# Kernel optimization log

Measured on AMD Instinct MI355X. Metric: run time of the kernel, lower is better.

The kernel has to match this reference:

```python
import jax, jax.numpy as jnp
import numpy as np

B, IN, N, D, O, H = 8192, 512, 16, 128, 256, 4
HD = D // H
PI = jnp.float32(np.pi)


def setup_inputs() -> dict:
    key = jax.random.key(0)
    ks = jax.random.split(key, 18)
    rn = lambda k, s, sc=1.0: jax.random.normal(k, s, dtype=jnp.float32) * sc
    return {
        'x': rn(ks[0], (B, IN)),
        'W_amp_r': rn(ks[1], (IN, N * D), 0.05), 'b_amp_r': rn(ks[2], (N * D,), 0.05),
        'W_amp_i': rn(ks[3], (IN, N * D), 0.05), 'b_amp_i': rn(ks[4], (N * D,), 0.05),
        'W_ph': rn(ks[5], (IN, N), 0.05), 'b_ph': rn(ks[6], (N,), 0.05),
        'A_param': rn(ks[7], (N, N), 0.01),
        'Wqkv_r': rn(ks[8], (D, 3 * D), 0.08), 'bqkv_r': rn(ks[9], (3 * D,), 0.08),
        'Wqkv_i': rn(ks[10], (D, 3 * D), 0.08), 'bqkv_i': rn(ks[11], (3 * D,), 0.08),
        'Wout_r': rn(ks[12], (D, D), 0.08), 'bout_r': rn(ks[13], (D,), 0.08),
        'Wout_i': rn(ks[14], (D, D), 0.08), 'bout_i': rn(ks[15], (D,), 0.08),
        'M_r': rn(ks[16], (N, D, O), 1.0 / np.sqrt(D)),
        'M_i': rn(ks[17], (N, D, O), 1.0 / np.sqrt(D)),
    }


def reference(x, W_amp_r, b_amp_r, W_amp_i, b_amp_i, W_ph, b_ph, A_param,
              Wqkv_r, bqkv_r, Wqkv_i, bqkv_i, Wout_r, bout_r, Wout_i, bout_i,
              M_r, M_i):
    # --- quantum phase encoding ---
    amp_r = (x @ W_amp_r + b_amp_r).reshape(B, N, D)
    amp_i = (x @ W_amp_i + b_amp_i).reshape(B, N, D)
    phases = jnp.tanh(x @ W_ph + b_ph) * PI                # (B, N)
    c, s = jnp.cos(phases)[..., None], jnp.sin(phases)[..., None]
    s_r = amp_r * c - amp_i * s
    s_i = amp_r * s + amp_i * c
    norm = jnp.sqrt(jnp.sum(s_r * s_r + s_i * s_i, -1, keepdims=True) + 1e-8)
    s_r, s_i = s_r / norm, s_i / norm
    # --- Cayley unitary interference ---
    A = (A_param - A_param.T).astype(jnp.complex64)
    I = jnp.eye(N, dtype=jnp.complex64)
    U = jnp.linalg.solve(I - 1j * A, I + 1j * A)           # (N, N) unitary
    st = (s_r + 1j * s_i).astype(jnp.complex64)
    interf = jnp.einsum('bmd,mn->bnd', st, U)
    sr, si = jnp.real(interf), jnp.imag(interf)
    # --- complex multi-head attention (magnitude softmax) ---
    scale = jnp.float32(HD ** -0.5)
    qkv_r = (sr @ Wqkv_r + bqkv_r).reshape(B, N, 3, H, HD).transpose(2, 0, 3, 1, 4)
    qkv_i = (si @ Wqkv_i + bqkv_i).reshape(B, N, 3, H, HD).transpose(2, 0, 3, 1, 4)
    q_r, k_r, v_r = qkv_r[0], qkv_r[1], qkv_r[2]
    q_i, k_i, v_i = qkv_i[0], qkv_i[1], qkv_i[2]
    ar = (jnp.einsum('bhnd,bhmd->bhnm', q_r, k_r) + jnp.einsum('bhnd,bhmd->bhnm', q_i, k_i)) * scale
    ai = (jnp.einsum('bhnd,bhmd->bhnm', q_i, k_r) - jnp.einsum('bhnd,bhmd->bhnm', q_r, k_i)) * scale
    w = jax.nn.softmax(jnp.sqrt(ar * ar + ai * ai), axis=-1)
    o_r = jnp.einsum('bhnm,bhmd->bhnd', w, v_r).transpose(0, 2, 1, 3).reshape(B, N, D)
    o_i = jnp.einsum('bhnm,bhmd->bhnd', w, v_i).transpose(0, 2, 1, 3).reshape(B, N, D)
    att_r = o_r @ Wout_r + bout_r
    att_i = o_i @ Wout_i + bout_i
    # --- quantum measurement ---
    m_r = jnp.einsum('bnd,ndo->bno', att_r, M_r) - jnp.einsum('bnd,ndo->bno', att_i, M_i)
    m_i = jnp.einsum('bnd,ndo->bno', att_r, M_i) + jnp.einsum('bnd,ndo->bno', att_i, M_r)
    probs = jax.nn.softmax(jnp.mean(jnp.sqrt(m_r * m_r + m_i * m_i), -1), axis=-1)  # (B, N)
    out_r = jnp.sum(m_r * probs[..., None], 1)
    out_i = jnp.sum(m_i * probs[..., None], 1)
    classical = jnp.sqrt(out_r * out_r + out_i * out_i)     # (B, O)
    # --- quantum metrics ---
    mag2 = sr * sr + si * si
    sum_sq = jnp.sum(mag2, -1)
    purity_bn = jnp.sum(mag2 * mag2, -1) / (sum_sq * sum_sq + 1e-8)
    purity_b = jnp.mean(purity_bn, -1)
    entanglement_b = -jnp.log(purity_b + 1e-8)
    fn = jnp.sqrt(jnp.sum(mag2, -1, keepdims=True) + 1e-8)
    nr, ni = sr / fn, si / fn
    Rij = jnp.einsum('bid,bjd->bij', nr, nr) + jnp.einsum('bid,bjd->bij', ni, ni)
    Iij = jnp.einsum('bid,bjd->bij', nr, ni) - jnp.einsum('bid,bjd->bij', ni, nr)
    fidelity = jnp.clip(Rij * Rij + Iij * Iij, 0.0, 1.0)    # (B, N, N), symmetric
    phase_var = jnp.mean(jnp.var(phases, axis=1, ddof=1))
    return (classical, probs, jnp.mean(att_r, 1), jnp.mean(att_i, 1),
            jnp.mean(purity_b), jnp.mean(entanglement_b), fidelity, phase_var)
```

## Files before the change

kernel.cpp:

```cpp
#include <hip/hip_runtime.h>
#include <math.h>

#define B_ 8192
#define IN_ 512
#define NQ 16
#define DD 128
#define OO 256
#define PI_F 3.14159274101257324f
#define INV_B (1.0f/8192.0f)
#define SCALE_F 0.176776695296636881f

#define OFF_CLASS 0
#define OFF_PROBS 2097152
#define OFF_ATTRM 2228224
#define OFF_ATTIM 3276800
#define OFF_PUR   4325376
#define OFF_ENT   4325377
#define OFF_FID   4325378
#define OFF_PV    6422530

__global__ __launch_bounds__(256) void cayley_kernel(const float* __restrict__ A_param,
                                                     float* __restrict__ Ur,
                                                     float* __restrict__ Ui) {
    __shared__ float Mr[16][17], Mi[16][17], Rr[16][17], Ri[16][17];
    const int t = threadIdx.x;
    const int r = t >> 4, c = t & 15;
    float a = A_param[r*16 + c] - A_param[c*16 + r];
    Mr[r][c] = (r == c) ? 1.0f : 0.0f;
    Mi[r][c] = -a;
    Rr[r][c] = (r == c) ? 1.0f : 0.0f;
    Ri[r][c] = a;
    __syncthreads();
    for (int p = 0; p < 16; p++) {
        float prr = Mr[p][p], pii = Mi[p][p];
        __syncthreads();
        if (r == p) {
            float inv = 1.0f / (prr*prr + pii*pii);
            float mr0 = Mr[p][c], mi0 = Mi[p][c];
            Mr[p][c] = (mr0*prr + mi0*pii) * inv;
            Mi[p][c] = (mi0*prr - mr0*pii) * inv;
            float rr0 = Rr[p][c], ri0 = Ri[p][c];
            Rr[p][c] = (rr0*prr + ri0*pii) * inv;
            Ri[p][c] = (ri0*prr - rr0*pii) * inv;
        }
        __syncthreads();
        float fr = Mr[r][p], fi = Mi[r][p];
        float mpr = Mr[p][c], mpi = Mi[p][c];
        float rpr = Rr[p][c], rpi = Ri[p][c];
        __syncthreads();
        if (r != p) {
            Mr[r][c] -= fr*mpr - fi*mpi;
            Mi[r][c] -= fr*mpi + fi*mpr;
            Rr[r][c] -= fr*rpr - fi*rpi;
            Ri[r][c] -= fr*rpi + fi*rpr;
        }
        __syncthreads();
    }
    Ur[t] = Rr[r][c];
    Ui[t] = Ri[r][c];
}

__global__ __launch_bounds__(256) void gemm_f32(const float* __restrict__ A, int lda,
                                                const float* __restrict__ W, int ldw,
                                                const float* __restrict__ bias,
                                                float* __restrict__ C, int ldc, int K) {
    __shared__ float As[32][132];
    __shared__ float Bs[32][132];
    const int t = threadIdx.x;
    const int tm = t >> 4, tn = t & 15;
    const size_t r0 = (size_t)blockIdx.x * 128;
    const int c0 = blockIdx.y * 128;
    float acc[8][8];
#pragma unroll
    for (int i = 0; i < 8; i++)
#pragma unroll
        for (int j = 0; j < 8; j++) acc[i][j] = 0.0f;

    for (int k0 = 0; k0 < K; k0 += 32) {
#pragma unroll
        for (int i = 0; i < 4; i++) {
            int idx = t + i*256;
            int mm = idx >> 3, kq = (idx & 7) << 2;
            float4 va = *(const float4*)&A[(r0 + mm)*lda + (k0 + kq)];
            As[kq+0][mm] = va.x; As[kq+1][mm] = va.y;
            As[kq+2][mm] = va.z; As[kq+3][mm] = va.w;
        }
#pragma unroll
        for (int i = 0; i < 4; i++) {
            int idx = t + i*256;
            int kk = idx >> 5, cq = (idx & 31) << 2;
            *(float4*)&Bs[kk][cq] = *(const float4*)&W[(size_t)(k0+kk)*ldw + (c0+cq)];
        }
        __syncthreads();
#pragma unroll
        for (int kk = 0; kk < 32; kk++) {
            float4 a0 = *(const float4*)&As[kk][tm*4];
            float4 a1 = *(const float4*)&As[kk][64 + tm*4];
            float4 b0 = *(const float4*)&Bs[kk][tn*4];
            float4 b1 = *(const float4*)&Bs[kk][64 + tn*4];
            float av[8] = {a0.x,a0.y,a0.z,a0.w,a1.x,a1.y,a1.z,a1.w};
            float bv[8] = {b0.x,b0.y,b0.z,b0.w,b1.x,b1.y,b1.z,b1.w};
#pragma unroll
            for (int i = 0; i < 8; i++)
#pragma unroll
                for (int j = 0; j < 8; j++)
                    acc[i][j] = fmaf(av[i], bv[j], acc[i][j]);
        }
        __syncthreads();
    }
#pragma unroll
    for (int ri = 0; ri < 2; ri++)
#pragma unroll
    for (int i = 0; i < 4; i++) {
        size_t row = r0 + ri*64 + tm*4 + i;
#pragma unroll
        for (int ci = 0; ci < 2; ci++) {
            int col = c0 + ci*64 + tn*4;
            float4 bb = *(const float4*)&bias[col];
            float4 v;
            v.x = acc[ri*4+i][ci*4+0] + bb.x;
            v.y = acc[ri*4+i][ci*4+1] + bb.y;
            v.z = acc[ri*4+i][ci*4+2] + bb.z;
            v.w = acc[ri*4+i][ci*4+3] + bb.w;
            *(float4*)&C[row*ldc + col] = v;
        }
    }
}

__global__ __launch_bounds__(256) void phases_kernel(const float* __restrict__ x,
                                                     const float* __restrict__ W_ph,
                                                     const float* __restrict__ b_ph,
                                                     float* __restrict__ phases) {
    __shared__ float xs[512];
    __shared__ float part[256];
    const int t = threadIdx.x;
    const size_t b = blockIdx.x;
    xs[t]       = x[b*512 + t];
    xs[t + 256] = x[b*512 + t + 256];
    __syncthreads();
    const int n2 = t & 15, g = t >> 4;
    float s = 0.0f;
#pragma unroll
    for (int j = 0; j < 32; j++) {
        int k = g*32 + j;
        s = fmaf(xs[k], W_ph[k*16 + n2], s);
    }
    part[t] = s;
    __syncthreads();
    if (t < 16) {
        float acc = b_ph[t];
#pragma unroll
        for (int g2 = 0; g2 < 16; g2++) acc += part[g2*16 + t];
        phases[b*16 + t] = tanhf(acc) * PI_F;
    }
}

__global__ __launch_bounds__(256) void mega_kernel(
    const float* ampR, const float* ampI,
    const float* __restrict__ phases,
    const float* __restrict__ Ur, const float* __restrict__ Ui,
    const float* __restrict__ Wqkv_r, const float* __restrict__ bqkv_r,
    const float* __restrict__ Wqkv_i, const float* __restrict__ bqkv_i,
    const float* __restrict__ Wout_r, const float* __restrict__ bout_r,
    const float* __restrict__ Wout_i, const float* __restrict__ bout_i,
    float* attR, float* attI,
    float* __restrict__ fid,
    float* __restrict__ attmR, float* __restrict__ attmI,
    float* __restrict__ pur_out, float* __restrict__ ent_out, float* __restrict__ pv_out)
{
    __shared__ float S[15808];
    float* br   = S;
    float* bi   = S + 2048;
    float* ir   = S + 4096;
    float* ii   = S + 6208;
    float* red  = S + 8320;
    float* red2 = S + 8576;
    float* csn  = S + 8832;
    float* snn  = S + 8848;
    float* invn = S + 8864;
    float* fnv  = S + 8880;
    float* purs = S + 8896;
    float* phl  = S + 8912;
    float* Urs  = S + 8928;
    float* Uis  = S + 9184;
    float* Wrc  = S + 9472;
    float* Wic  = S + 12544;
    float* qr2  = S;
    float* qi2  = S + 2112;
    float* kr2  = S + 4224;
    float* ki2  = S + 6336;
    float* vr2  = S + 8448;
    float* vi2  = S + 10560;
    float* wbuf = S + 12672;
    float* Wor  = S + 13760;
    float* Woi  = S + 14784;
    float* or_  = S;
    float* oi_  = S + 2112;
    float* attSr= S + 4224;
    float* attSi= S + 6336;

    const int t = threadIdx.x;
    const size_t b = blockIdx.x;

    {
        const float4* aR = (const float4*)(ampR + b*2048);
        const float4* aI = (const float4*)(ampI + b*2048);
#pragma unroll
        for (int i = 0; i < 2; i++) {
            int c = t + i*256;
            *(float4*)&br[c*4] = aR[c];
            *(float4*)&bi[c*4] = aI[c];
        }
    }
    Urs[t] = Ur[t]; Uis[t] = Ui[t];
    if (t < 16) {
        float p = phases[b*16 + t];
        phl[t] = p; csn[t] = cosf(p); snn[t] = sinf(p);
    }
    __syncthreads();
#pragma unroll
    for (int i = 0; i < 8; i++) {
        int idx = t + i*256;
        int n2 = idx >> 7;
        float ar = br[idx], ai = bi[idx];
        float cc = csn[n2], ss = snn[n2];
        br[idx] = ar*cc - ai*ss;
        bi[idx] = ar*ss + ai*cc;
    }
    __syncthreads();
    {
        const int n2 = t >> 4, g = t & 15;
        const float* pr  = &br[n2*128 + g*8];
        const float* pi2 = &bi[n2*128 + g*8];
        float s = 0.0f;
#pragma unroll
        for (int j = 0; j < 8; j++) s += pr[j]*pr[j] + pi2[j]*pi2[j];
        red[t] = s;
    }
    __syncthreads();
    if (t < 16) {
        float s = 0.0f;
#pragma unroll
        for (int g2 = 0; g2 < 16; g2++) s += red[t*16 + g2];
        invn[t] = 1.0f / sqrtf(s + 1e-8f);
    }
    __syncthreads();
#pragma unroll
    for (int i = 0; i < 8; i++) {
        int idx = t + i*256;
        float iv = invn[idx >> 7];
        br[idx] *= iv; bi[idx] *= iv;
    }
    __syncthreads();
#pragma unroll
    for (int rep = 0; rep < 8; rep++) {
        int o = t + rep*256;
        int n2 = o >> 7, d = o & 127;
        float ar = 0.0f, ai = 0.0f;
#pragma unroll
        for (int m = 0; m < 16; m++) {
            float vr = br[m*128 + d], vi = bi[m*128 + d];
            float ur = Urs[m*16 + n2], ui = Uis[m*16 + n2];
            ar += vr*ur - vi*ui;
            ai += vr*ui + vi*ur;
        }
        ir[n2*132 + d] = ar; ii[n2*132 + d] = ai;
    }
    __syncthreads();
    {
        const int n2 = t >> 4, g = t & 15;
        float s2 = 0.0f, s4 = 0.0f;
#pragma unroll
        for (int j = 0; j < 8; j++) {
            float xr = ir[n2*132 + g*8+j], xi = ii[n2*132 + g*8+j];
            float m2 = xr*xr + xi*xi;
            s2 += m2; s4 += m2*m2;
        }
        red[t] = s2; red2[t] = s4;
    }
    __syncthreads();
    if (t < 16) {
        float S2 = 0.0f, S4 = 0.0f;
#pragma unroll
        for (int g2 = 0; g2 < 16; g2++) { S2 += red[t*16+g2]; S4 += red2[t*16+g2]; }
        purs[t] = S4 / (S2*S2 + 1e-8f);
        fnv[t] = sqrtf(S2 + 1e-8f);
    }
    __syncthreads();
    if (t == 0) {
        float pb = 0.0f;
#pragma unroll
        for (int n2 = 0; n2 < 16; n2++) pb += purs[n2];
        pb *= (1.0f/16.0f);
        atomicAdd(pur_out, pb * INV_B);
        atomicAdd(ent_out, -logf(pb + 1e-8f) * INV_B);
    }
    if (t == 1) {
        float mean = 0.0f;
#pragma unroll
        for (int n2 = 0; n2 < 16; n2++) mean += phl[n2];
        mean *= (1.0f/16.0f);
        float var = 0.0f;
#pragma unroll
        for (int n2 = 0; n2 < 16; n2++) { float dv = phl[n2] - mean; var += dv*dv; }
        var *= (1.0f/15.0f);
        atomicAdd(pv_out, var * INV_B);
    }
    {
        const int i2 = t >> 4, j2 = t & 15;
        float Rt = 0.0f, It = 0.0f;
#pragma unroll
        for (int d0 = 0; d0 < 128; d0 += 4) {
            float4 xr = *(const float4*)&ir[i2*132 + d0];
            float4 xi = *(const float4*)&ii[i2*132 + d0];
            float4 yr = *(const float4*)&ir[j2*132 + d0];
            float4 yi = *(const float4*)&ii[j2*132 + d0];
            Rt += xr.x*yr.x + xi.x*yi.x;  It += xr.x*yi.x - xi.x*yr.x;
            Rt += xr.y*yr.y + xi.y*yi.y;  It += xr.y*yi.y - xi.y*yr.y;
            Rt += xr.z*yr.z + xi.z*yi.z;  It += xr.z*yi.z - xi.z*yr.z;
            Rt += xr.w*yr.w + xi.w*yi.w;  It += xr.w*yi.w - xi.w*yr.w;
        }
        float inv = 1.0f / (fnv[i2]*fnv[j2]);
        float F = (Rt*Rt + It*It) * inv * inv;
        F = fminf(fmaxf(F, 0.0f), 1.0f);
        fid[b*256 + t] = F;
    }

    const int cg = t >> 4, nn = t & 15;
    float aq[24], bq[24];
#pragma unroll
    for (int j = 0; j < 24; j++) { aq[j] = 0.0f; bq[j] = 0.0f; }
    for (int d0 = 0; d0 < 128; d0 += 8) {
        __syncthreads();
#pragma unroll
        for (int i = 0; i < 3; i++) {
            int idx = (t + i*256) * 4;
            *(float4*)&Wrc[idx] = *(const float4*)&Wqkv_r[d0*384 + idx];
            *(float4*)&Wic[idx] = *(const float4*)&Wqkv_i[d0*384 + idx];
        }
        __syncthreads();
#pragma unroll
        for (int dd = 0; dd < 8; dd++) {
            const float arr = ir[nn*132 + d0 + dd];
            const float aii = ii[nn*132 + d0 + dd];
#pragma unroll
            for (int s2 = 0; s2 < 6; s2++) {
                const float4 wr4 = *(const float4*)&Wrc[dd*384 + cg*4 + 64*s2];
                const float4 wi4 = *(const float4*)&Wic[dd*384 + cg*4 + 64*s2];
                aq[s2*4+0] = fmaf(arr, wr4.x, aq[s2*4+0]);
                aq[s2*4+1] = fmaf(arr, wr4.y, aq[s2*4+1]);
                aq[s2*4+2] = fmaf(arr, wr4.z, aq[s2*4+2]);
                aq[s2*4+3] = fmaf(arr, wr4.w, aq[s2*4+3]);
                bq[s2*4+0] = fmaf(aii, wi4.x, bq[s2*4+0]);
                bq[s2*4+1] = fmaf(aii, wi4.y, bq[s2*4+1]);
                bq[s2*4+2] = fmaf(aii, wi4.z, bq[s2*4+2]);
                bq[s2*4+3] = fmaf(aii, wi4.w, bq[s2*4+3]);
            }
        }
    }
    __syncthreads();
#pragma unroll
    for (int s2 = 0; s2 < 6; s2++) {
#pragma unroll
        for (int j = 0; j < 4; j++) {
            const int c = cg*4 + 64*s2 + j;
            float qvr = aq[s2*4+j] + bqkv_r[c];
            float qvi = bq[s2*4+j] + bqkv_i[c];
            if (s2 < 2)      { qr2[nn*132 + c]         = qvr; qi2[nn*132 + c]         = qvi; }
            else if (s2 < 4) { kr2[nn*132 + (c-128)]   = qvr; ki2[nn*132 + (c-128)]   = qvi; }
            else             { vr2[nn*132 + (c-256)]   = qvr; vi2[nn*132 + (c-256)]   = qvi; }
        }
    }
    __syncthreads();

    {
        const int nq = t >> 4, m = t & 15;
#pragma unroll
        for (int h = 0; h < 4; h++) {
            float ar = 0.0f, ai = 0.0f;
            const int bqo = h*32;
#pragma unroll
            for (int d0 = 0; d0 < 32; d0 += 4) {
                float4 q_r = *(const float4*)&qr2[nq*132 + bqo + d0];
                float4 k_r = *(const float4*)&kr2[m*132  + bqo + d0];
                float4 q_i = *(const float4*)&qi2[nq*132 + bqo + d0];
                float4 k_i = *(const float4*)&ki2[m*132  + bqo + d0];
                ar += q_r.x*k_r.x + q_i.x*k_i.x + q_r.y*k_r.y + q_i.y*k_i.y
                    + q_r.z*k_r.z + q_i.z*k_i.z + q_r.w*k_r.w + q_i.w*k_i.w;
                ai += q_i.x*k_r.x - q_r.x*k_i.x + q_i.y*k_r.y - q_r.y*k_i.y
                    + q_i.z*k_r.z - q_r.z*k_i.z + q_i.w*k_r.w - q_r.w*k_i.w;
            }
            wbuf[h*272 + nq*17 + m] = sqrtf(ar*ar + ai*ai) * SCALE_F;
        }
    }
    __syncthreads();
    if (t < 64) {
        const int h = t >> 4, n2 = t & 15;
        float* row = &wbuf[h*272 + n2*17];
        float mx = row[0];
#pragma unroll
        for (int k = 1; k < 16; k++) mx = fmaxf(mx, row[k]);
        float ev[16];
        float sum = 0.0f;
#pragma unroll
        for (int k = 0; k < 16; k++) { ev[k] = expf(row[k] - mx); sum += ev[k]; }
        float inv = 1.0f / sum;
#pragma unroll
        for (int k = 0; k < 16; k++) row[k] = ev[k] * inv;
    }
    __syncthreads();

    {
        const int og = t >> 4, n2 = t & 15;
        const int hh = og >> 2;
        float por[8] = {0,0,0,0,0,0,0,0}, poi[8] = {0,0,0,0,0,0,0,0};
#pragma unroll
        for (int m2 = 0; m2 < 16; m2++) {
            float w = wbuf[hh*272 + n2*17 + m2];
            float4 v0 = *(const float4*)&vr2[m2*132 + og*8];
            float4 v1 = *(const float4*)&vr2[m2*132 + og*8 + 4];
            float4 u0 = *(const float4*)&vi2[m2*132 + og*8];
            float4 u1 = *(const float4*)&vi2[m2*132 + og*8 + 4];
            por[0] = fmaf(w, v0.x, por[0]); por[1] = fmaf(w, v0.y, por[1]);
            por[2] = fmaf(w, v0.z, por[2]); por[3] = fmaf(w, v0.w, por[3]);
            por[4] = fmaf(w, v1.x, por[4]); por[5] = fmaf(w, v1.y, por[5]);
            por[6] = fmaf(w, v1.z, por[6]); por[7] = fmaf(w, v1.w, por[7]);
            poi[0] = fmaf(w, u0.x, poi[0]); poi[1] = fmaf(w, u0.y, poi[1]);
            poi[2] = fmaf(w, u0.z, poi[2]); poi[3] = fmaf(w, u0.w, poi[3]);
            poi[4] = fmaf(w, u1.x, poi[4]); poi[5] = fmaf(w, u1.y, poi[5]);
            poi[6] = fmaf(w, u1.z, poi[6]); poi[7] = fmaf(w, u1.w, poi[7]);
        }
#pragma unroll
        for (int j = 0; j < 8; j++) {
            or_[n2*132 + og*8 + j] = por[j];
            oi_[n2*132 + og*8 + j] = poi[j];
        }
    }
    __syncthreads();

    {
        const int og = t >> 4, n2 = t & 15;
        float atr[8] = {0,0,0,0,0,0,0,0}, ati[8] = {0,0,0,0,0,0,0,0};
        for (int d0 = 0; d0 < 128; d0 += 8) {
            __syncthreads();
            *(float4*)&Wor[t*4] = *(const float4*)&Wout_r[d0*128 + t*4];
            *(float4*)&Woi[t*4] = *(const float4*)&Wout_i[d0*128 + t*4];
            __syncthreads();
#pragma unroll
            for (int dd = 0; dd < 8; dd++) {
                const float a_r = or_[n2*132 + d0 + dd];
                const float a_i = oi_[n2*132 + d0 + dd];
                float4 w0 = *(const float4*)&Wor[dd*128 + og*8];
                float4 w1 = *(const float4*)&Wor[dd*128 + og*8 + 4];
                float4 u0 = *(const float4*)&Woi[dd*128 + og*8];
                float4 u1 = *(const float4*)&Woi[dd*128 + og*8 + 4];
                atr[0] = fmaf(a_r, w0.x, atr[0]); atr[1] = fmaf(a_r, w0.y, atr[1]);
                atr[2] = fmaf(a_r, w0.z, atr[2]); atr[3] = fmaf(a_r, w0.w, atr[3]);
                atr[4] = fmaf(a_r, w1.x, atr[4]); atr[5] = fmaf(a_r, w1.y, atr[5]);
                atr[6] = fmaf(a_r, w1.z, atr[6]); atr[7] = fmaf(a_r, w1.w, atr[7]);
                ati[0] = fmaf(a_i, u0.x, ati[0]); ati[1] = fmaf(a_i, u0.y, ati[1]);
                ati[2] = fmaf(a_i, u0.z, ati[2]); ati[3] = fmaf(a_i, u0.w, ati[3]);
                ati[4] = fmaf(a_i, u1.x, ati[4]); ati[5] = fmaf(a_i, u1.y, ati[5]);
                ati[6] = fmaf(a_i, u1.z, ati[6]); ati[7] = fmaf(a_i, u1.w, ati[7]);
            }
        }
        const float4 br0 = *(const float4*)&bout_r[og*8];
        const float4 br1 = *(const float4*)&bout_r[og*8 + 4];
        const float4 bi0 = *(const float4*)&bout_i[og*8];
        const float4 bi1 = *(const float4*)&bout_i[og*8 + 4];
        float4 o0 = make_float4(atr[0]+br0.x, atr[1]+br0.y, atr[2]+br0.z, atr[3]+br0.w);
        float4 o1 = make_float4(atr[4]+br1.x, atr[5]+br1.y, atr[6]+br1.z, atr[7]+br1.w);
        float4 e0 = make_float4(ati[0]+bi0.x, ati[1]+bi0.y, ati[2]+bi0.z, ati[3]+bi0.w);
        float4 e1 = make_float4(ati[4]+bi1.x, ati[5]+bi1.y, ati[6]+bi1.z, ati[7]+bi1.w);
        size_t gbase = b*2048 + (size_t)n2*128 + og*8;
        *(float4*)&attR[gbase]     = o0;
        *(float4*)&attR[gbase + 4] = o1;
        *(float4*)&attI[gbase]     = e0;
        *(float4*)&attI[gbase + 4] = e1;
        *(float4*)&attSr[n2*132 + og*8]     = o0;
        *(float4*)&attSr[n2*132 + og*8 + 4] = o1;
        *(float4*)&attSi[n2*132 + og*8]     = e0;
        *(float4*)&attSi[n2*132 + og*8 + 4] = e1;
    }
    __syncthreads();

    if (t < 128) {
        const int d = t;
        float s = 0.0f;
#pragma unroll
        for (int n2 = 0; n2 < 16; n2++) s += attSr[n2*132 + d];
        attmR[b*128 + d] = s * (1.0f/16.0f);
    } else {
        const int d = t - 128;
        float s = 0.0f;
#pragma unroll
        for (int n2 = 0; n2 < 16; n2++) s += attSi[n2*132 + d];
        attmI[b*128 + d] = s * (1.0f/16.0f);
    }
}

template<int MODE>
__global__ __launch_bounds__(256) void measure_kernel(const float* __restrict__ attR,
                                                      const float* __restrict__ attI,
                                                      const float* __restrict__ M_r,
                                                      const float* __restrict__ M_i,
                                                      float* __restrict__ mR,
                                                      float* __restrict__ mI,
                                                      float* __restrict__ mag,
                                                      const float* __restrict__ probs,
                                                      float* __restrict__ orAcc,
                                                      float* __restrict__ oiAcc) {
    __shared__ float ar_s[32*128];
    __shared__ float ai_s[32*128];
    const int t = threadIdx.x;
    const size_t b0 = (size_t)blockIdx.x * 32;
    const int n = blockIdx.y;
#pragma unroll
    for (int i = 0; i < 4; i++) {
        int c = t + i*256;
        int row = c >> 5, d4 = (c & 31) << 2;
        *(float4*)&ar_s[row*128 + d4] = *(const float4*)&attR[((b0+row)*16 + n)*128 + d4];
        *(float4*)&ai_s[row*128 + d4] = *(const float4*)&attI[((b0+row)*16 + n)*128 + d4];
    }
    __syncthreads();
    const int ol = t & 63;
    const int rg = t >> 6;
    const int obase = ol * 4;
    float mr[8][4], mi[8][4];
#pragma unroll
    for (int i = 0; i < 8; i++)
#pragma unroll
        for (int j = 0; j < 4; j++) { mr[i][j] = 0.0f; mi[i][j] = 0.0f; }
    const float* Mrp = M_r + (size_t)n*DD*OO;
    const float* Mip = M_i + (size_t)n*DD*OO;
    for (int k0 = 0; k0 < 128; k0 += 4) {
        float4 Mr4[4], Mi4[4];
#pragma unroll
        for (int u = 0; u < 4; u++) {
            Mr4[u] = *(const float4*)&Mrp[(k0+u)*256 + obase];
            Mi4[u] = *(const float4*)&Mip[(k0+u)*256 + obase];
        }
#pragma unroll
        for (int r8 = 0; r8 < 8; r8++) {
            const int row = rg*8 + r8;
            float4 a4 = *(const float4*)&ar_s[row*128 + k0];
            float4 c4 = *(const float4*)&ai_s[row*128 + k0];
            float arv[4] = {a4.x, a4.y, a4.z, a4.w};
            float aiv[4] = {c4.x, c4.y, c4.z, c4.w};
#pragma unroll
            for (int u = 0; u < 4; u++) {
                float ar = arv[u], ai = aiv[u];
                mr[r8][0] = fmaf(ar, Mr4[u].x, mr[r8][0]); mr[r8][0] = fmaf(-ai, Mi4[u].x, mr[r8][0]);
                mr[r8][1] = fmaf(ar, Mr4[u].y, mr[r8][1]); mr[r8][1] = fmaf(-ai, Mi4[u].y, mr[r8][1]);
                mr[r8][2] = fmaf(ar, Mr4[u].z, mr[r8][2]); mr[r8][2] = fmaf(-ai, Mi4[u].z, mr[r8][2]);
                mr[r8][3] = fmaf(ar, Mr4[u].w, mr[r8][3]); mr[r8][3] = fmaf(-ai, Mi4[u].w, mr[r8][3]);
                mi[r8][0] = fmaf(ar, Mi4[u].x, mi[r8][0]); mi[r8][0] = fmaf( ai, Mr4[u].x, mi[r8][0]);
                mi[r8][1] = fmaf(ar, Mi4[u].y, mi[r8][1]); mi[r8][1] = fmaf( ai, Mr4[u].y, mi[r8][1]);
                mi[r8][2] = fmaf(ar, Mi4[u].z, mi[r8][2]); mi[r8][2] = fmaf( ai, Mr4[u].z, mi[r8][2]);
                mi[r8][3] = fmaf(ar, Mi4[u].w, mi[r8][3]); mi[r8][3] = fmaf( ai, Mr4[u].w, mi[r8][3]);
            }
        }
    }
#pragma unroll
    for (int r8 = 0; r8 < 8; r8++) {
        const int row = rg*8 + r8;
        if constexpr (MODE == 0) {
            size_t base = ((b0+row)*16 + n)*256 + obase;
            *(float4*)&mR[base] = make_float4(mr[r8][0], mr[r8][1], mr[r8][2], mr[r8][3]);
            *(float4*)&mI[base] = make_float4(mi[r8][0], mi[r8][1], mi[r8][2], mi[r8][3]);
        }
        if constexpr (MODE == 2) {
            float p = probs[(b0+row)*16 + n];
            size_t abase = (b0+row)*256 + obase;
#pragma unroll
            for (int u = 0; u < 4; u++) {
                atomicAdd(&orAcc[abase + u], p * mr[r8][u]);
                atomicAdd(&oiAcc[abase + u], p * mi[r8][u]);
            }
        } else {
            float p = 0.0f;
#pragma unroll
            for (int u = 0; u < 4; u++)
                p += sqrtf(mr[r8][u]*mr[r8][u] + mi[r8][u]*mi[r8][u]);
#pragma unroll
            for (int s = 32; s > 0; s >>= 1) p += __shfl_down(p, s, 64);
            if (ol == 0) mag[(b0+row)*16 + n] = p * (1.0f/256.0f);
        }
    }
}

__global__ __launch_bounds__(256) void final_kernel(const float* __restrict__ mR,
                                                    const float* __restrict__ mI,
                                                    const float* __restrict__ mag,
                                                    float* __restrict__ cls,
                                                    float* __restrict__ probs) {
    __shared__ float pr[16];
    const size_t b = blockIdx.x;
    const int t = threadIdx.x;
    if (t == 0) {
        float v[16];
        float mx = -1e30f;
#pragma unroll
        for (int n2 = 0; n2 < 16; n2++) { v[n2] = mag[b*16 + n2]; mx = fmaxf(mx, v[n2]); }
        float sum = 0.0f;
#pragma unroll
        for (int n2 = 0; n2 < 16; n2++) { float e = expf(v[n2] - mx); pr[n2] = e; sum += e; }
        float inv = 1.0f / sum;
#pragma unroll
        for (int n2 = 0; n2 < 16; n2++) pr[n2] *= inv;
    }
    __syncthreads();
    if (t < 16) probs[b*16 + t] = pr[t];
    float orv = 0.0f, oiv = 0.0f;
#pragma unroll
    for (int n2 = 0; n2 < 16; n2++) {
        float p = pr[n2];
        size_t base = (b*16 + n2)*256 + t;
        orv = fmaf(mR[base], p, orv);
        oiv = fmaf(mI[base], p, oiv);
    }
    cls[b*256 + t] = sqrtf(orv*orv + oiv*oiv);
}

__global__ __launch_bounds__(256) void probs_kernel(const float* __restrict__ mag,
                                                    float* __restrict__ probs) {
    const int b = blockIdx.x*256 + threadIdx.x;
    float v[16];
    float mx = -1e30f;
#pragma unroll
    for (int n2 = 0; n2 < 16; n2++) { v[n2] = mag[b*16 + n2]; mx = fmaxf(mx, v[n2]); }
    float sum = 0.0f;
#pragma unroll
    for (int n2 = 0; n2 < 16; n2++) { v[n2] = expf(v[n2] - mx); sum += v[n2]; }
    float inv = 1.0f / sum;
#pragma unroll
    for (int n2 = 0; n2 < 16; n2++) probs[b*16 + n2] = v[n2] * inv;
}

__global__ __launch_bounds__(256) void classical_kernel(const float* __restrict__ orAcc,
                                                        const float* __restrict__ oiAcc,
                                                        float* __restrict__ cls) {
    const size_t i = (size_t)blockIdx.x*256 + threadIdx.x;
    float a = orAcc[i], c = oiAcc[i];
    cls[i] = sqrtf(a*a + c*c);
}

extern "C" void kernel_launch(void* const* d_in, const int* in_sizes, int n_in,
                              void* d_out, int out_size, void* d_ws, size_t ws_size,
                              hipStream_t stream) {
    const float* x        = (const float*)d_in[0];
    const float* W_amp_r  = (const float*)d_in[1];
    const float* b_amp_r  = (const float*)d_in[2];
    const float* W_amp_i  = (const float*)d_in[3];
    const float* b_amp_i  = (const float*)d_in[4];
    const float* W_ph     = (const float*)d_in[5];
    const float* b_ph     = (const float*)d_in[6];
    const float* A_param  = (const float*)d_in[7];
    const float* Wqkv_r   = (const float*)d_in[8];
    const float* bqkv_r   = (const float*)d_in[9];
    const float* Wqkv_i   = (const float*)d_in[10];
    const float* bqkv_i   = (const float*)d_in[11];
    const float* Wout_r   = (const float*)d_in[12];
    const float* bout_r   = (const float*)d_in[13];
    const float* Wout_i   = (const float*)d_in[14];
    const float* bout_i   = (const float*)d_in[15];
    const float* M_r      = (const float*)d_in[16];
    const float* M_i      = (const float*)d_in[17];
    float* out = (float*)d_out;
    float* ws  = (float*)d_ws;

    float* ampR = ws;
    float* ampI = ws + 16777216;
    float* attR = ampR;
    float* attI = ampI;

    const bool big = ws_size >= (size_t)403703808ull;
    float *mRp = nullptr, *mIp = nullptr, *orA = nullptr, *oiA = nullptr;
    float *phases, *mag, *UrP, *UiP;
    if (big) {
        mRp    = ws + 33554432;
        mIp    = ws + 67108864;
        phases = ws + 100663296;
        mag    = ws + 100794368;
        UrP    = ws + 100925440;
        UiP    = ws + 100925696;
    } else {
        orA    = ws + 33554432;
        oiA    = ws + 35651584;
        phases = ws + 37748736;
        mag    = ws + 37879808;
        UrP    = ws + 38010880;
        UiP    = ws + 38011136;
    }

    hipMemsetAsync(out + OFF_PUR, 0, 2*sizeof(float), stream);
    hipMemsetAsync(out + OFF_PV,  0, sizeof(float), stream);
    if (!big) hipMemsetAsync(orA, 0, 2ull*2097152ull*sizeof(float), stream);

    cayley_kernel<<<1, 256, 0, stream>>>(A_param, UrP, UiP);

    gemm_f32<<<dim3(64, 16), 256, 0, stream>>>(x, 512, W_amp_r, 2048, b_amp_r, ampR, 2048, 512);
    gemm_f32<<<dim3(64, 16), 256, 0, stream>>>(x, 512, W_amp_i, 2048, b_amp_i, ampI, 2048, 512);
    phases_kernel<<<8192, 256, 0, stream>>>(x, W_ph, b_ph, phases);

    mega_kernel<<<8192, 256, 0, stream>>>(ampR, ampI, phases, UrP, UiP,
                                          Wqkv_r, bqkv_r, Wqkv_i, bqkv_i,
                                          Wout_r, bout_r, Wout_i, bout_i,
                                          attR, attI,
                                          out + OFF_FID, out + OFF_ATTRM, out + OFF_ATTIM,
                                          out + OFF_PUR, out + OFF_ENT, out + OFF_PV);

    if (big) {
        measure_kernel<0><<<dim3(256, 16), 256, 0, stream>>>(attR, attI, M_r, M_i,
                                                             mRp, mIp, mag, nullptr, nullptr, nullptr);
        final_kernel<<<8192, 256, 0, stream>>>(mRp, mIp, mag, out + OFF_CLASS, out + OFF_PROBS);
    } else {
        measure_kernel<1><<<dim3(256, 16), 256, 0, stream>>>(attR, attI, M_r, M_i,
                                                             nullptr, nullptr, mag, nullptr, nullptr, nullptr);
        probs_kernel<<<32, 256, 0, stream>>>(mag, out + OFF_PROBS);
        measure_kernel<2><<<dim3(256, 16), 256, 0, stream>>>(attR, attI, M_r, M_i,
                                                             nullptr, nullptr, nullptr,
                                                             out + OFF_PROBS, orA, oiA);
        classical_kernel<<<8192, 256, 0, stream>>>(orA, oiA, out + OFF_CLASS);
    }
}
```

Measured before the change: 3.305 ms.

## Replace atomic classical accumulation with fused weighted measurement kernel; shrink mega_kernel LDS

Removes the big-workspace path that materialised full m_r/m_i tensors, along with the small path's atomicAdd accumulation. In their place, a single recompute pass (wclass_kernel) redoes the measurement GEMM per batch tile, weights it by probs and writes the classical output directly. The mega_kernel shared-memory footprint is reduced by aliasing buffers, halving the QKV weight chunk and using a 130 stride, and it now requests 3 blocks per CU for occupancy. The cost is recomputing the measurement GEMM twice, plus a possible register-pressure risk from the launch bound.

```diff
diff --git a/kernel.cpp b/kernel.cpp
--- a/kernel.cpp
+++ b/kernel.cpp
@@ -155,7 +155,7 @@
     }
 }
 
-__global__ __launch_bounds__(256) void mega_kernel(
+__global__ __launch_bounds__(256, 3) void mega_kernel(
     const float* ampR, const float* ampI,
     const float* __restrict__ phases,
     const float* __restrict__ Ur, const float* __restrict__ Ui,
@@ -168,11 +168,11 @@
     float* __restrict__ attmR, float* __restrict__ attmI,
     float* __restrict__ pur_out, float* __restrict__ ent_out, float* __restrict__ pv_out)
 {
-    __shared__ float S[15808];
-    float* br   = S;
-    float* bi   = S + 2048;
-    float* ir   = S + 4096;
-    float* ii   = S + 6208;
+    __shared__ float S[13568];
+    float* ir   = S;
+    float* ii   = S + 2112;
+    float* br   = S + 4224;
+    float* bi   = S + 6272;
     float* red  = S + 8320;
     float* red2 = S + 8576;
     float* csn  = S + 8832;
@@ -183,21 +183,21 @@
     float* phl  = S + 8912;
     float* Urs  = S + 8928;
     float* Uis  = S + 9184;
-    float* Wrc  = S + 9472;
-    float* Wic  = S + 12544;
+    float* Wrc  = S + 4224;
+    float* Wic  = S + 5760;
     float* qr2  = S;
-    float* qi2  = S + 2112;
-    float* kr2  = S + 4224;
-    float* ki2  = S + 6336;
-    float* vr2  = S + 8448;
-    float* vi2  = S + 10560;
-    float* wbuf = S + 12672;
-    float* Wor  = S + 13760;
-    float* Woi  = S + 14784;
+    float* qi2  = S + 2080;
+    float* kr2  = S + 4160;
+    float* ki2  = S + 6240;
+    float* vr2  = S + 8320;
+    float* vi2  = S + 10400;
+    float* wbuf = S + 12480;
     float* or_  = S;
-    float* oi_  = S + 2112;
-    float* attSr= S + 4224;
-    float* attSi= S + 6336;
+    float* oi_  = S + 2080;
+    float* Wor  = S + 4160;
+    float* Woi  = S + 5184;
+    float* attSr= S + 8320;
+    float* attSi= S + 10400;
 
     const int t = threadIdx.x;
     const size_t b = blockIdx.x;
@@ -330,17 +330,17 @@
     float aq[24], bq[24];
 #pragma unroll
     for (int j = 0; j < 24; j++) { aq[j] = 0.0f; bq[j] = 0.0f; }
-    for (int d0 = 0; d0 < 128; d0 += 8) {
-        __syncthreads();
-#pragma unroll
-        for (int i = 0; i < 3; i++) {
-            int idx = (t + i*256) * 4;
-            *(float4*)&Wrc[idx] = *(const float4*)&Wqkv_r[d0*384 + idx];
-            *(float4*)&Wic[idx] = *(const float4*)&Wqkv_i[d0*384 + idx];
-        }
-        __syncthreads();
-#pragma unroll
-        for (int dd = 0; dd < 8; dd++) {
+    for (int d0 = 0; d0 < 128; d0 += 4) {
+        __syncthreads();
+#pragma unroll
+        for (int i = 0; i < 6; i++) {
+            int idx = t + i*256;
+            Wrc[idx] = Wqkv_r[d0*384 + idx];
+            Wic[idx] = Wqkv_i[d0*384 + idx];
+        }
+        __syncthreads();
+#pragma unroll
+        for (int dd = 0; dd < 4; dd++) {
             const float arr = ir[nn*132 + d0 + dd];
             const float aii = ii[nn*132 + d0 + dd];
 #pragma unroll
@@ -366,9 +366,9 @@
             const int c = cg*4 + 64*s2 + j;
             float qvr = aq[s2*4+j] + bqkv_r[c];
             float qvi = bq[s2*4+j] + bqkv_i[c];
-            if (s2 < 2)      { qr2[nn*132 + c]         = qvr; qi2[nn*132 + c]         = qvi; }
-            else if (s2 < 4) { kr2[nn*132 + (c-128)]   = qvr; ki2[nn*132 + (c-128)]   = qvi; }
-            else             { vr2[nn*132 + (c-256)]   = qvr; vi2[nn*132 + (c-256)]   = qvi; }
+            if (s2 < 2)      { qr2[nn*130 + c]         = qvr; qi2[nn*130 + c]         = qvi; }
+            else if (s2 < 4) { kr2[nn*130 + (c-128)]   = qvr; ki2[nn*130 + (c-128)]   = qvi; }
+            else             { vr2[nn*130 + (c-256)]   = qvr; vi2[nn*130 + (c-256)]   = qvi; }
         }
     }
     __syncthreads();
@@ -381,10 +381,10 @@
             const int bqo = h*32;
 #pragma unroll
             for (int d0 = 0; d0 < 32; d0 += 4) {
-                float4 q_r = *(const float4*)&qr2[nq*132 + bqo + d0];
-                float4 k_r = *(const float4*)&kr2[m*132  + bqo + d0];
-                float4 q_i = *(const float4*)&qi2[nq*132 + bqo + d0];
-                float4 k_i = *(const float4*)&ki2[m*132  + bqo + d0];
+                float4 q_r = *(const float4*)&qr2[nq*130 + bqo + d0];
+                float4 k_r = *(const float4*)&kr2[m*130  + bqo + d0];
+                float4 q_i = *(const float4*)&qi2[nq*130 + bqo + d0];
+                float4 k_i = *(const float4*)&ki2[m*130  + bqo + d0];
                 ar += q_r.x*k_r.x + q_i.x*k_i.x + q_r.y*k_r.y + q_i.y*k_i.y
                     + q_r.z*k_r.z + q_i.z*k_i.z + q_r.w*k_r.w + q_i.w*k_i.w;
                 ai += q_i.x*k_r.x - q_r.x*k_i.x + q_i.y*k_r.y - q_r.y*k_i.y
@@ -417,10 +417,10 @@
 #pragma unroll
         for (int m2 = 0; m2 < 16; m2++) {
             float w = wbuf[hh*272 + n2*17 + m2];
-            float4 v0 = *(const float4*)&vr2[m2*132 + og*8];
-            float4 v1 = *(const float4*)&vr2[m2*132 + og*8 + 4];
-            float4 u0 = *(const float4*)&vi2[m2*132 + og*8];
-            float4 u1 = *(const float4*)&vi2[m2*132 + og*8 + 4];
+            float4 v0 = *(const float4*)&vr2[m2*130 + og*8];
+            float4 v1 = *(const float4*)&vr2[m2*130 + og*8 + 4];
+            float4 u0 = *(const float4*)&vi2[m2*130 + og*8];
+            float4 u1 = *(const float4*)&vi2[m2*130 + og*8 + 4];
             por[0] = fmaf(w, v0.x, por[0]); por[1] = fmaf(w, v0.y, por[1]);
             por[2] = fmaf(w, v0.z, por[2]); por[3] = fmaf(w, v0.w, por[3]);
             por[4] = fmaf(w, v1.x, por[4]); por[5] = fmaf(w, v1.y, por[5]);
@@ -430,13 +430,13 @@
             poi[4] = fmaf(w, u1.x, poi[4]); poi[5] = fmaf(w, u1.y, poi[5]);
             poi[6] = fmaf(w, u1.z, poi[6]); poi[7] = fmaf(w, u1.w, poi[7]);
         }
+        __syncthreads();
 #pragma unroll
         for (int j = 0; j < 8; j++) {
-            or_[n2*132 + og*8 + j] = por[j];
-            oi_[n2*132 + og*8 + j] = poi[j];
-        }
-    }
-    __syncthreads();
+            or_[n2*130 + og*8 + j] = por[j];
+            oi_[n2*130 + og*8 + j] = poi[j];
+        }
+    }
 
     {
         const int og = t >> 4, n2 = t & 15;
@@ -448,8 +448,8 @@
             __syncthreads();
 #pragma unroll
             for (int dd = 0; dd < 8; dd++) {
-                const float a_r = or_[n2*132 + d0 + dd];
-                const float a_i = oi_[n2*132 + d0 + dd];
+                const float a_r = or_[n2*130 + d0 + dd];
+                const float a_i = oi_[n2*130 + d0 + dd];
                 float4 w0 = *(const float4*)&Wor[dd*128 + og*8];
                 float4 w1 = *(const float4*)&Wor[dd*128 + og*8 + 4];
                 float4 u0 = *(const float4*)&Woi[dd*128 + og*8];
@@ -477,10 +477,10 @@
         *(float4*)&attR[gbase + 4] = o1;
         *(float4*)&attI[gbase]     = e0;
         *(float4*)&attI[gbase + 4] = e1;
-        *(float4*)&attSr[n2*132 + og*8]     = o0;
-        *(float4*)&attSr[n2*132 + og*8 + 4] = o1;
-        *(float4*)&attSi[n2*132 + og*8]     = e0;
-        *(float4*)&attSi[n2*132 + og*8 + 4] = e1;
+        *(float4*)&attSr[n2*130 + og*8]     = o0;
+        *(float4*)&attSr[n2*130 + og*8 + 4] = o1;
+        *(float4*)&attSi[n2*130 + og*8]     = e0;
+        *(float4*)&attSi[n2*130 + og*8 + 4] = e1;
     }
     __syncthreads();
 
@@ -488,28 +488,22 @@
         const int d = t;
         float s = 0.0f;
 #pragma unroll
-        for (int n2 = 0; n2 < 16; n2++) s += attSr[n2*132 + d];
+        for (int n2 = 0; n2 < 16; n2++) s += attSr[n2*130 + d];
         attmR[b*128 + d] = s * (1.0f/16.0f);
     } else {
         const int d = t - 128;
         float s = 0.0f;
 #pragma unroll
-        for (int n2 = 0; n2 < 16; n2++) s += attSi[n2*132 + d];
+        for (int n2 = 0; n2 < 16; n2++) s += attSi[n2*130 + d];
         attmI[b*128 + d] = s * (1.0f/16.0f);
     }
 }
 
-template<int MODE>
-__global__ __launch_bounds__(256) void measure_kernel(const float* __restrict__ attR,
-                                                      const float* __restrict__ attI,
-                                                      const float* __restrict__ M_r,
-                                                      const float* __restrict__ M_i,
-                                                      float* __restrict__ mR,
-                                                      float* __restrict__ mI,
-                                                      float* __restrict__ mag,
-                                                      const float* __restrict__ probs,
-                                                      float* __restrict__ orAcc,
-                                                      float* __restrict__ oiAcc) {
+__global__ __launch_bounds__(256) void mag_kernel(const float* __restrict__ attR,
+                                                  const float* __restrict__ attI,
+                                                  const float* __restrict__ M_r,
+                                                  const float* __restrict__ M_i,
+                                                  float* __restrict__ mag) {
     __shared__ float ar_s[32*128];
     __shared__ float ai_s[32*128];
     const int t = threadIdx.x;
@@ -564,62 +558,14 @@
 #pragma unroll
     for (int r8 = 0; r8 < 8; r8++) {
         const int row = rg*8 + r8;
-        if constexpr (MODE == 0) {
-            size_t base = ((b0+row)*16 + n)*256 + obase;
-            *(float4*)&mR[base] = make_float4(mr[r8][0], mr[r8][1], mr[r8][2], mr[r8][3]);
-            *(float4*)&mI[base] = make_float4(mi[r8][0], mi[r8][1], mi[r8][2], mi[r8][3]);
-        }
-        if constexpr (MODE == 2) {
-            float p = probs[(b0+row)*16 + n];
-            size_t abase = (b0+row)*256 + obase;
-#pragma unroll
-            for (int u = 0; u < 4; u++) {
-                atomicAdd(&orAcc[abase + u], p * mr[r8][u]);
-                atomicAdd(&oiAcc[abase + u], p * mi[r8][u]);
-            }
-        } else {
-            float p = 0.0f;
-#pragma unroll
-            for (int u = 0; u < 4; u++)
-                p += sqrtf(mr[r8][u]*mr[r8][u] + mi[r8][u]*mi[r8][u]);
-#pragma unroll
-            for (int s = 32; s > 0; s >>= 1) p += __shfl_down(p, s, 64);
-            if (ol == 0) mag[(b0+row)*16 + n] = p * (1.0f/256.0f);
-        }
-    }
-}
-
-__global__ __launch_bounds__(256) void final_kernel(const float* __restrict__ mR,
-                                                    const float* __restrict__ mI,
-                                                    const float* __restrict__ mag,
-                                                    float* __restrict__ cls,
-                                                    float* __restrict__ probs) {
-    __shared__ float pr[16];
-    const size_t b = blockIdx.x;
-    const int t = threadIdx.x;
-    if (t == 0) {
-        float v[16];
-        float mx = -1e30f;
-#pragma unroll
-        for (int n2 = 0; n2 < 16; n2++) { v[n2] = mag[b*16 + n2]; mx = fmaxf(mx, v[n2]); }
-        float sum = 0.0f;
-#pragma unroll
-        for (int n2 = 0; n2 < 16; n2++) { float e = expf(v[n2] - mx); pr[n2] = e; sum += e; }
-        float inv = 1.0f / sum;
-#pragma unroll
-        for (int n2 = 0; n2 < 16; n2++) pr[n2] *= inv;
-    }
-    __syncthreads();
-    if (t < 16) probs[b*16 + t] = pr[t];
-    float orv = 0.0f, oiv = 0.0f;
-#pragma unroll
-    for (int n2 = 0; n2 < 16; n2++) {
-        float p = pr[n2];
-        size_t base = (b*16 + n2)*256 + t;
-        orv = fmaf(mR[base], p, orv);
-        oiv = fmaf(mI[base], p, oiv);
-    }
-    cls[b*256 + t] = sqrtf(orv*orv + oiv*oiv);
+        float p = 0.0f;
+#pragma unroll
+        for (int u = 0; u < 4; u++)
+            p += sqrtf(mr[r8][u]*mr[r8][u] + mi[r8][u]*mi[r8][u]);
+#pragma unroll
+        for (int s = 32; s > 0; s >>= 1) p += __shfl_down(p, s, 64);
+        if (ol == 0) mag[(b0+row)*16 + n] = p * (1.0f/256.0f);
+    }
 }
 
 __global__ __launch_bounds__(256) void probs_kernel(const float* __restrict__ mag,
@@ -637,12 +583,90 @@
     for (int n2 = 0; n2 < 16; n2++) probs[b*16 + n2] = v[n2] * inv;
 }
 
-__global__ __launch_bounds__(256) void classical_kernel(const float* __restrict__ orAcc,
-                                                        const float* __restrict__ oiAcc,
+__global__ __launch_bounds__(512, 4) void wclass_kernel(const float* __restrict__ attR,
+                                                        const float* __restrict__ attI,
+                                                        const float* __restrict__ M_r,
+                                                        const float* __restrict__ M_i,
+                                                        const float* __restrict__ probs,
                                                         float* __restrict__ cls) {
-    const size_t i = (size_t)blockIdx.x*256 + threadIdx.x;
-    float a = orAcc[i], c = oiAcc[i];
-    cls[i] = sqrtf(a*a + c*c);
+    __shared__ float ar_s[16*128];
+    __shared__ float ai_s[16*128];
+    __shared__ float p_s[256];
+    const int t = threadIdx.x;
+    const size_t b0 = (size_t)blockIdx.x * 16;
+    const int ol = t & 63;
+    const int rg = t >> 6;
+    const int obase = ol * 4;
+    float aor[2][4], aoi[2][4];
+#pragma unroll
+    for (int r2 = 0; r2 < 2; r2++)
+#pragma unroll
+        for (int u = 0; u < 4; u++) { aor[r2][u] = 0.0f; aoi[r2][u] = 0.0f; }
+    if (t < 256) p_s[t] = probs[b0*16 + t];
+
+    for (int n = 0; n < 16; n++) {
+        __syncthreads();
+        {
+            int row = t >> 5, d4 = (t & 31) << 2;
+            *(float4*)&ar_s[row*128 + d4] = *(const float4*)&attR[((b0+row)*16 + n)*128 + d4];
+            *(float4*)&ai_s[row*128 + d4] = *(const float4*)&attI[((b0+row)*16 + n)*128 + d4];
+        }
+        __syncthreads();
+        float mr[2][4], mi[2][4];
+#pragma unroll
+        for (int r2 = 0; r2 < 2; r2++)
+#pragma unroll
+            for (int u = 0; u < 4; u++) { mr[r2][u] = 0.0f; mi[r2][u] = 0.0f; }
+        const float* Mrp = M_r + (size_t)n*DD*OO;
+        const float* Mip = M_i + (size_t)n*DD*OO;
+        for (int k0 = 0; k0 < 128; k0 += 4) {
+            float4 Mr4[4], Mi4[4];
+#pragma unroll
+            for (int u = 0; u < 4; u++) {
+                Mr4[u] = *(const float4*)&Mrp[(k0+u)*256 + obase];
+                Mi4[u] = *(const float4*)&Mip[(k0+u)*256 + obase];
+            }
+#pragma unroll
+            for (int r2 = 0; r2 < 2; r2++) {
+                const int row = rg*2 + r2;
+                float4 a4 = *(const float4*)&ar_s[row*128 + k0];
+                float4 c4 = *(const float4*)&ai_s[row*128 + k0];
+                float arv[4] = {a4.x, a4.y, a4.z, a4.w};
+                float aiv[4] = {c4.x, c4.y, c4.z, c4.w};
+#pragma unroll
+                for (int u = 0; u < 4; u++) {
+                    float ar = arv[u], ai = aiv[u];
+                    mr[r2][0] = fmaf(ar, Mr4[u].x, mr[r2][0]); mr[r2][0] = fmaf(-ai, Mi4[u].x, mr[r2][0]);
+                    mr[r2][1] = fmaf(ar, Mr4[u].y, mr[r2][1]); mr[r2][1] = fmaf(-ai, Mi4[u].y, mr[r2][1]);
+                    mr[r2][2] = fmaf(ar, Mr4[u].z, mr[r2][2]); mr[r2][2] = fmaf(-ai, Mi4[u].z, mr[r2][2]);
+                    mr[r2][3] = fmaf(ar, Mr4[u].w, mr[r2][3]); mr[r2][3] = fmaf(-ai, Mi4[u].w, mr[r2][3]);
+                    mi[r2][0] = fmaf(ar, Mi4[u].x, mi[r2][0]); mi[r2][0] = fmaf( ai, Mr4[u].x, mi[r2][0]);
+                    mi[r2][1] = fmaf(ar, Mi4[u].y, mi[r2][1]); mi[r2][1] = fmaf( ai, Mr4[u].y, mi[r2][1]);
+                    mi[r2][2] = fmaf(ar, Mi4[u].z, mi[r2][2]); mi[r2][2] = fmaf( ai, Mr4[u].z, mi[r2][2]);
+                    mi[r2][3] = fmaf(ar, Mi4[u].w, mi[r2][3]); mi[r2][3] = fmaf( ai, Mr4[u].w, mi[r2][3]);
+                }
+            }
+        }
+#pragma unroll
+        for (int r2 = 0; r2 < 2; r2++) {
+            float p = p_s[(rg*2 + r2)*16 + n];
+#pragma unroll
+            for (int u = 0; u < 4; u++) {
+                aor[r2][u] = fmaf(p, mr[r2][u], aor[r2][u]);
+                aoi[r2][u] = fmaf(p, mi[r2][u], aoi[r2][u]);
+            }
+        }
+    }
+#pragma unroll
+    for (int r2 = 0; r2 < 2; r2++) {
+        const int row = rg*2 + r2;
+        float4 o;
+        o.x = sqrtf(aor[r2][0]*aor[r2][0] + aoi[r2][0]*aoi[r2][0]);
+        o.y = sqrtf(aor[r2][1]*aor[r2][1] + aoi[r2][1]*aoi[r2][1]);
+        o.z = sqrtf(aor[r2][2]*aor[r2][2] + aoi[r2][2]*aoi[r2][2]);
+        o.w = sqrtf(aor[r2][3]*aor[r2][3] + aoi[r2][3]*aoi[r2][3]);
+        *(float4*)&cls[(b0+row)*256 + obase] = o;
+    }
 }
 
 extern "C" void kernel_launch(void* const* d_in, const int* in_sizes, int n_in,
@@ -669,33 +693,17 @@
     float* out = (float*)d_out;
     float* ws  = (float*)d_ws;
 
-    float* ampR = ws;
-    float* ampI = ws + 16777216;
-    float* attR = ampR;
-    float* attI = ampI;
-
-    const bool big = ws_size >= (size_t)403703808ull;
-    float *mRp = nullptr, *mIp = nullptr, *orA = nullptr, *oiA = nullptr;
-    float *phases, *mag, *UrP, *UiP;
-    if (big) {
-        mRp    = ws + 33554432;
-        mIp    = ws + 67108864;
-        phases = ws + 100663296;
-        mag    = ws + 100794368;
-        UrP    = ws + 100925440;
-        UiP    = ws + 100925696;
-    } else {
-        orA    = ws + 33554432;
-        oiA    = ws + 35651584;
-        phases = ws + 37748736;
-        mag    = ws + 37879808;
-        UrP    = ws + 38010880;
-        UiP    = ws + 38011136;
-    }
+    float* ampR   = ws;
+    float* ampI   = ws + 16777216;
+    float* attR   = ampR;
+    float* attI   = ampI;
+    float* phases = ws + 33554432;
+    float* mag    = ws + 33685504;
+    float* UrP    = ws + 33816576;
+    float* UiP    = ws + 33816832;
 
     hipMemsetAsync(out + OFF_PUR, 0, 2*sizeof(float), stream);
     hipMemsetAsync(out + OFF_PV,  0, sizeof(float), stream);
-    if (!big) hipMemsetAsync(orA, 0, 2ull*2097152ull*sizeof(float), stream);
 
     cayley_kernel<<<1, 256, 0, stream>>>(A_param, UrP, UiP);
 
@@ -710,17 +718,7 @@
                                           out + OFF_FID, out + OFF_ATTRM, out + OFF_ATTIM,
                                           out + OFF_PUR, out + OFF_ENT, out + OFF_PV);
 
-    if (big) {
-        measure_kernel<0><<<dim3(256, 16), 256, 0, stream>>>(attR, attI, M_r, M_i,
-                                                             mRp, mIp, mag, nullptr, nullptr, nullptr);
-        final_kernel<<<8192, 256, 0, stream>>>(mRp, mIp, mag, out + OFF_CLASS, out + OFF_PROBS);
-    } else {
-        measure_kernel<1><<<dim3(256, 16), 256, 0, stream>>>(attR, attI, M_r, M_i,
-                                                             nullptr, nullptr, mag, nullptr, nullptr, nullptr);
-        probs_kernel<<<32, 256, 0, stream>>>(mag, out + OFF_PROBS);
-        measure_kernel<2><<<dim3(256, 16), 256, 0, stream>>>(attR, attI, M_r, M_i,
-                                                             nullptr, nullptr, nullptr,
-                                                             out + OFF_PROBS, orA, oiA);
-        classical_kernel<<<8192, 256, 0, stream>>>(orA, oiA, out + OFF_CLASS);
-    }
+    mag_kernel<<<dim3(256, 16), 256, 0, stream>>>(attR, attI, M_r, M_i, mag);
+    probs_kernel<<<32, 256, 0, stream>>>(mag, out + OFF_PROBS);
+    wclass_kernel<<<512, 512, 0, stream>>>(attR, attI, M_r, M_i, out + OFF_PROBS, out + OFF_CLASS);
 }
```

Result: faster. 3.207 ms (-3.0%).
